# Optimization experiments

Measured on AMD Instinct MI355X. Metric: run time of the kernel, lower is better.

The kernel has to match this reference:

```python
import jax, jax.numpy as jnp
import numpy as np

N = 65536          # total nodes across batch
C = 256            # in channels
COUT = 256         # out channels
B = 8              # batch size (graphs)
EMB = 512          # emb channels
N_EDGE_TYPE = 7
N_NODE_TYPE = 7
AVG_DEGREE = 7
E = N * AVG_DEGREE
GROUP = 32         # min(32, channels)
EPS = 1e-5


def setup_inputs() -> dict:
    key = jax.random.key(0)
    ks = jax.random.split(key, 10)
    # GraphConv init: uniform xavier-like with fan scaled by avg_degree
    std = (2.0 / float(AVG_DEGREE * C + AVG_DEGREE * COUT)) ** 0.5
    a = (3.0 ** 0.5) * std
    return {
        "x": jax.random.normal(ks[0], (N, C), jnp.float32),
        "emb": jax.random.normal(ks[1], (B, EMB), jnp.float32),
        "batch_id": jnp.sort(jax.random.randint(ks[2], (N,), 0, B, jnp.int32)),
        "edge_index": jax.random.randint(ks[3], (2, E), 0, N, jnp.int32),
        "edge_type": jax.random.randint(ks[4], (E,), 0, N_EDGE_TYPE, jnp.int32),
        "node_type": jax.random.randint(ks[5], (N,), 0, N_NODE_TYPE, jnp.int32),
        "gn1_w": jnp.ones((1, C), jnp.float32),
        "gn1_b": jnp.zeros((1, C), jnp.float32),
        "conv1_w": jax.random.uniform(ks[6], (N_EDGE_TYPE * (C + N_NODE_TYPE), COUT), jnp.float32, -a, a),
        "emb_w": jax.random.normal(ks[7], (EMB, COUT), jnp.float32) * 0.02,
        "emb_b": jnp.zeros((COUT,), jnp.float32),
        "gn2_w": jnp.ones((1, COUT), jnp.float32),
        "gn2_b": jnp.zeros((1, COUT), jnp.float32),
        "conv2_w": jax.random.uniform(ks[8], (N_EDGE_TYPE * (COUT + N_NODE_TYPE), COUT), jnp.float32, -a, a),
    }


def _adjust_for_group(t, cpg):
    # sum stats within each group of cpg channels, broadcast back: [B, C]
    if cpg > 1:
        Bsz, Cn = t.shape
        g = Cn // cpg
        t = t.reshape(Bsz, g, cpg).sum(-1, keepdims=True)
        t = jnp.broadcast_to(t, (Bsz, g, cpg)).reshape(Bsz, Cn)
    return t


def dual_octree_group_norm(data, batch_id, w, b):
    # data: [N, C]; per-graph group norm via segment sums
    Cn = data.shape[1]
    cpg = Cn // GROUP
    ones = jnp.ones((data.shape[0], 1), data.dtype)
    count = jax.ops.segment_sum(ones, batch_id, num_segments=B) * cpg   # [B,1]
    inv_count = 1.0 / (count + EPS)
    mean = jax.ops.segment_sum(data, batch_id, num_segments=B) * inv_count
    mean = _adjust_for_group(mean, cpg)
    out = data - mean[batch_id]
    var = jax.ops.segment_sum(out * out, batch_id, num_segments=B) * inv_count
    var = _adjust_for_group(var, cpg)
    inv_std = 1.0 / jnp.sqrt(var + EPS)
    out = out * inv_std[batch_id]
    return out * w + b


def graph_conv(x, weights, edge_index, edge_type, node_type):
    # concat one-hot node type channels
    one_hot = jax.nn.one_hot(node_type, N_NODE_TYPE, dtype=x.dtype)
    xa = jnp.concatenate([x, one_hot], axis=1)          # [N, C+T]
    row, col = edge_index[0], edge_index[1]
    index = row * N_EDGE_TYPE + edge_type               # [E]
    col_data = jax.ops.segment_sum(xa[col], index, num_segments=xa.shape[0] * N_EDGE_TYPE)
    return col_data.reshape(xa.shape[0], -1) @ weights  # [N, COUT]


def reference(x, emb, batch_id, edge_index, edge_type, node_type,
              gn1_w, gn1_b, conv1_w, emb_w, emb_b, gn2_w, gn2_b, conv2_w):
    h = dual_octree_group_norm(x, batch_id, gn1_w, gn1_b)
    h = jax.nn.silu(h)
    h = graph_conv(h, conv1_w, edge_index, edge_type, node_type)
    emb_out = jax.nn.silu(emb) @ emb_w + emb_b          # [B, COUT]
    h = h + emb_out[batch_id]                           # per-batch add (loop in torch)
    h = dual_octree_group_norm(h, batch_id, gn2_w, gn2_b)
    h = jax.nn.silu(h)                                  # dropout p=0 -> identity
    h = graph_conv(h, conv2_w, edge_index, edge_type, node_type)
    return x + h                                        # skip is Identity (Cout==C)
```

## Files before the change

### kernel.cpp

```cpp
#include <hip/hip_runtime.h>
#include <math.h>

#define N_NODES 65536
#define B_GR    8
#define EMB_N   512
#define E_EDGES 458752
#define NSEG    458752
#define TSTRIDE 288
#define GK      2016
#define EPS     1e-5f

typedef unsigned short u16;
typedef unsigned int   u32;
typedef __bf16 bf16x8 __attribute__((ext_vector_type(8)));
typedef float  f32x4  __attribute__((ext_vector_type(4)));
typedef u16    u16x8  __attribute__((ext_vector_type(8)));

__device__ __forceinline__ float bf2f(u16 u) {
    u32 x = ((u32)u) << 16; float f; __builtin_memcpy(&f, &x, 4); return f;
}
__device__ __forceinline__ u16 f2bf(float f) {
    u32 x; __builtin_memcpy(&x, &f, 4);
    u32 r = x + 0x7fffu + ((x >> 16) & 1u);
    return (u16)(r >> 16);
}

__device__ __forceinline__ void stats_body(int nb, int tid, const float* __restrict__ xin,
                                           const int* __restrict__ batch_id,
                                           float* __restrict__ S, float* __restrict__ Q) {
    int c = tid;
    int n0 = nb * 64;
    float s = 0.f, q = 0.f;
    int bcur = batch_id[n0];
    for (int r = 0; r < 64; r++) {
        int n = n0 + r;
        int b = batch_id[n];
        if (b != bcur) {
            atomicAdd(&S[bcur * 256 + c], s);
            atomicAdd(&Q[bcur * 256 + c], q);
            s = 0.f; q = 0.f; bcur = b;
        }
        float v = xin[(size_t)n * 256 + c];
        s += v;
        q = fmaf(v, v, q);
    }
    atomicAdd(&S[bcur * 256 + c], s);
    atomicAdd(&Q[bcur * 256 + c], q);
}

__device__ __forceinline__ void norm_body(int nb, int tid, const float* __restrict__ xin,
                                          const int* __restrict__ batch_id,
                                          const float* __restrict__ S, const float* __restrict__ Q,
                                          const int* __restrict__ cnt,
                                          const float* __restrict__ w, const float* __restrict__ bias,
                                          u16* __restrict__ yout) {
    __shared__ float smean[256], sistd[256];
    {
        int b = tid >> 5, g = tid & 31;
        float Sg = 0.f, Qg = 0.f;
#pragma unroll
        for (int k = 0; k < 8; k++) {
            Sg += S[b * 256 + g * 8 + k];
            Qg += Q[b * 256 + g * 8 + k];
        }
        float cnt8 = (float)cnt[b] * 8.f;
        float D = cnt8 + EPS;
        float m = Sg / D;
        float var = (Qg - 2.f * m * Sg + cnt8 * m * m) / D;
        smean[tid] = m;
        sistd[tid] = rsqrtf(var + EPS);
    }
    __syncthreads();
    int n = nb * 8 + (tid >> 5);
    int g = tid & 31;
    int c0 = g * 8;
    int b = batch_id[n];
    float m = smean[b * 32 + g], is = sistd[b * 32 + g];
    u16x8 o;
#pragma unroll
    for (int k = 0; k < 8; k++) {
        float v = (xin[(size_t)n * 256 + c0 + k] - m) * is;
        v = v * w[c0 + k] + bias[c0 + k];
        v = v / (1.f + __expf(-v));
        o[k] = f2bf(v);
    }
    *(u16x8*)&yout[(size_t)n * 256 + c0] = o;
}

__global__ __launch_bounds__(256) void front_kernel(
    const int* __restrict__ batch_id, int* __restrict__ cnt,
    const float* __restrict__ w1, const float* __restrict__ w2,
    u16* __restrict__ Wt1, u16* __restrict__ Wt2,
    const float* __restrict__ emb, const float* __restrict__ embw,
    const float* __restrict__ embb, float* __restrict__ embout,
    const float* __restrict__ x, float* __restrict__ S, float* __restrict__ Q)
{
    int bid = blockIdx.x, tid = threadIdx.x;
    if (bid < 256) {
        int i = bid * 256 + tid;
        int b = batch_id[i];
#pragma unroll
        for (int bb = 0; bb < 8; bb++) {
            unsigned long long mm = __ballot(b == bb);
            if ((tid & 63) == 0 && mm) atomicAdd(&cnt[bb], (int)__popcll(mm));
        }
    } else if (bid < 1264) {
        int r = bid - 256;
        const float* Win = (r < 504) ? w1 : w2;
        u16* Wt = (r < 504) ? Wt1 : Wt2;
        r %= 504;
        int t  = r / 72;
        int r2 = r % 72;
        int cc0 = (r2 / 8) * 32;
        int n0  = (r2 % 8) * 32;
        __shared__ float tile[32][33];
        int cl = tid & 31, rh = tid >> 5;
#pragma unroll
        for (int rr = 0; rr < 4; rr++) {
            int c = cc0 + rh + rr * 8;
            float v = 0.f;
            if (c < 263) v = Win[(size_t)(t * 263 + c) * 256 + n0 + cl];
            tile[rh + rr * 8][cl] = v;
        }
        __syncthreads();
#pragma unroll
        for (int rr = 0; rr < 4; rr++) {
            int n = n0 + rh + rr * 8;
            Wt[(size_t)n * GK + t * TSTRIDE + cc0 + cl] = f2bf(tile[cl][rh + rr * 8]);
        }
    } else if (bid == 1264) {
        __shared__ float semb[B_GR * EMB_N];
        for (int i = tid; i < B_GR * EMB_N; i += 256) {
            float e = emb[i];
            semb[i] = e / (1.f + __expf(-e));
        }
        __syncthreads();
        float acc[8];
        float bb = embb[tid];
#pragma unroll
        for (int b = 0; b < 8; b++) acc[b] = bb;
        for (int k = 0; k < EMB_N; k++) {
            float wv = embw[k * 256 + tid];
#pragma unroll
            for (int b = 0; b < 8; b++) acc[b] += semb[b * EMB_N + k] * wv;
        }
#pragma unroll
        for (int b = 0; b < 8; b++) embout[b * 256 + tid] = acc[b];
    } else {
        stats_body(bid - 1265, tid, x, batch_id, S, Q);
    }
}

__global__ __launch_bounds__(256) void hist_norm_kernel(
    const int* __restrict__ ei, const int* __restrict__ et, int* __restrict__ hist,
    const float* __restrict__ xin, const int* __restrict__ batch_id,
    const float* __restrict__ S, const float* __restrict__ Q, const int* __restrict__ cnt,
    const float* __restrict__ w, const float* __restrict__ bias, u16* __restrict__ yout)
{
    int bid = blockIdx.x;
    if (bid < 1792) {
        int e = bid * 256 + threadIdx.x;
        int s = ei[e] * 7 + et[e];
        atomicAdd(&hist[s], 1);
    } else {
        norm_body(bid - 1792, threadIdx.x, xin, batch_id, S, Q, cnt, w, bias, yout);
    }
}

__global__ __launch_bounds__(256) void stats_kernel(const float* __restrict__ xin,
                                                    const int* __restrict__ batch_id,
                                                    float* __restrict__ S, float* __restrict__ Q) {
    stats_body(blockIdx.x, threadIdx.x, xin, batch_id, S, Q);
}
__global__ __launch_bounds__(256) void norm_kernel(const float* __restrict__ xin,
                                                   const int* __restrict__ batch_id,
                                                   const float* __restrict__ S, const float* __restrict__ Q,
                                                   const int* __restrict__ cnt,
                                                   const float* __restrict__ w, const float* __restrict__ bias,
                                                   u16* __restrict__ yout) {
    norm_body(blockIdx.x, threadIdx.x, xin, batch_id, S, Q, cnt, w, bias, yout);
}

__global__ __launch_bounds__(512) void scan1_kernel(const int* __restrict__ hist, int* __restrict__ partials) {
    __shared__ int sd[512];
    int i = blockIdx.x * 512 + threadIdx.x;
    sd[threadIdx.x] = hist[i];
    __syncthreads();
    for (int off = 256; off > 0; off >>= 1) {
        if (threadIdx.x < off) sd[threadIdx.x] += sd[threadIdx.x + off];
        __syncthreads();
    }
    if (threadIdx.x == 0) partials[blockIdx.x] = sd[0];
}

__global__ __launch_bounds__(1024) void scan2_kernel(int* __restrict__ partials) {
    __shared__ int sd[1024];
    int t = threadIdx.x;
    int v = (t < 896) ? partials[t] : 0;
    sd[t] = v;
    __syncthreads();
    for (int off = 1; off < 1024; off <<= 1) {
        int u = (t >= off) ? sd[t - off] : 0;
        __syncthreads();
        sd[t] += u;
        __syncthreads();
    }
    if (t < 896) partials[t] = sd[t] - v;
}

__global__ __launch_bounds__(512) void scan3_kernel(int* __restrict__ hist_offs, const int* __restrict__ partials,
                                                    int* __restrict__ cursor) {
    __shared__ int sd[512];
    int t = threadIdx.x;
    int i = blockIdx.x * 512 + t;
    int c = hist_offs[i];
    sd[t] = c;
    __syncthreads();
    for (int off = 1; off < 512; off <<= 1) {
        int u = (t >= off) ? sd[t - off] : 0;
        __syncthreads();
        sd[t] += u;
        __syncthreads();
    }
    int o = partials[blockIdx.x] + sd[t] - c;
    hist_offs[i] = o;
    cursor[i] = o;
}

__global__ __launch_bounds__(256) void fill_zero_kernel(const int* __restrict__ ei, const int* __restrict__ et,
                                                        int* __restrict__ cursor, int* __restrict__ elist,
                                                        float* __restrict__ S, float* __restrict__ Q) {
    int bid = blockIdx.x;
    if (bid < 1792) {
        int e = bid * 256 + threadIdx.x;
        int s = ei[e] * 7 + et[e];
        int p = atomicAdd(&cursor[s], 1);
        if (p >= 0 && p < E_EDGES) elist[p] = ei[E_EDGES + e];
    } else {
        int i = (bid - 1792) * 256 + threadIdx.x;
        S[i] = 0.f; Q[i] = 0.f;
    }
}

__global__ __launch_bounds__(512) void gemm_fused_kernel(
    const u16* __restrict__ y, const u16* __restrict__ Bt,
    const int* __restrict__ offs, const int* __restrict__ cursor,
    const int* __restrict__ elist, const int* __restrict__ node_type,
    const int* __restrict__ batch_id, const float* __restrict__ embout,
    const float* __restrict__ xres, float* __restrict__ out, int mode)
{
    __shared__ __align__(16) u16 As[2][64 * 64];
    int tid = threadIdx.x;
    int lane = tid & 63;
    int wn = tid >> 6;
    int lm = lane & 15, lq = lane >> 4;
    int m0 = blockIdx.x * 64;
    int ar = tid >> 3;
    int tq = tid & 7;

    f32x4 acc[4][2];
    f32x4 zz = {0.f, 0.f, 0.f, 0.f};
#pragma unroll
    for (int i = 0; i < 4; i++)
#pragma unroll
        for (int j = 0; j < 2; j++) acc[i][j] = zz;

    const u16* btp0 = Bt + (size_t)(wn * 32 + lm) * GK + lq * 8;
    const u16* btp1 = btp0 + (size_t)16 * GK;

    int sbase = (m0 + ar) * 7;

    int st = offs[sbase], en = cursor[sbase];
    int col[4];
#pragma unroll
    for (int u = 0; u < 4; u++) col[u] = (st + u < en) ? elist[st + u] : -1;
    u16x8 gv[4];
#pragma unroll
    for (int u = 0; u < 4; u++)
        if (col[u] >= 0) gv[u] = *(const u16x8*)&y[(size_t)col[u] * 256 + tq * 8];
    bf16x8 bcur[2][2];
#pragma unroll
    for (int k = 0; k < 2; k++) {
        bcur[k][0] = *(const bf16x8*)&btp0[k * 32];
        bcur[k][1] = *(const bf16x8*)&btp1[k * 32];
    }
    bf16x8 boh[2];
    int stn = 0, enn = 0;
    int coln[4] = {-1, -1, -1, -1};
    int nt4[4] = {-1, -1, -1, -1};
    int buf = 0;

    for (int t = 0; t < 7; t++) {
#pragma unroll
        for (int sc = 0; sc < 4; sc++) {
            float f[8];
#pragma unroll
            for (int j = 0; j < 8; j++) f[j] = 0.f;
#pragma unroll
            for (int u = 0; u < 4; u++)
                if (col[u] >= 0) {
#pragma unroll
                    for (int j = 0; j < 8; j++) f[j] += bf2f(gv[u][j]);
                }
            if (en - st > 4) {
                for (int e = st + 4; e < en; e++) {
                    u16x8 v = *(const u16x8*)&y[(size_t)elist[e] * 256 + sc * 64 + tq * 8];
#pragma unroll
                    for (int j = 0; j < 8; j++) f[j] += bf2f(v[j]);
                }
            }
            {
                u16x8 w8;
#pragma unroll
                for (int j = 0; j < 8; j++) w8[j] = f2bf(f[j]);
                *(u16x8*)&As[buf][ar * 64 + ((tq ^ (ar & 7)) * 8)] = w8;
            }
            __syncthreads();
            bf16x8 a[2][4];
#pragma unroll
            for (int k = 0; k < 2; k++)
#pragma unroll
                for (int i = 0; i < 4; i++) {
                    int row = i * 16 + lm;
                    a[k][i] = *(const bf16x8*)&As[buf][row * 64 + (((k * 4 + lq) ^ (row & 7)) * 8)];
                }
            bf16x8 bn00, bn01, bn10, bn11;
            if (sc < 3) {
                int cb = (sc + 1) * 64 + tq * 8;
#pragma unroll
                for (int u = 0; u < 4; u++)
                    if (col[u] >= 0) gv[u] = *(const u16x8*)&y[(size_t)col[u] * 256 + cb];
                int kb = t * TSTRIDE + (sc + 1) * 64;
                bn00 = *(const bf16x8*)&btp0[kb];
                bn01 = *(const bf16x8*)&btp1[kb];
                bn10 = *(const bf16x8*)&btp0[kb + 32];
                bn11 = *(const bf16x8*)&btp1[kb + 32];
                if (sc == 0 && t < 6) { stn = offs[sbase + t + 1]; enn = cursor[sbase + t + 1]; }
                if (sc == 1 && t < 6) {
#pragma unroll
                    for (int u = 0; u < 4; u++) coln[u] = (stn + u < enn) ? elist[stn + u] : -1;
                }
                if (sc == 2 && tq == 0) {
#pragma unroll
                    for (int u = 0; u < 4; u++) nt4[u] = (col[u] >= 0) ? node_type[col[u]] : -1;
                }
            } else {
                int kb = t * TSTRIDE + 256;
                boh[0] = *(const bf16x8*)&btp0[kb];
                boh[1] = *(const bf16x8*)&btp1[kb];
                if (t < 6) {
#pragma unroll
                    for (int u = 0; u < 4; u++)
                        if (coln[u] >= 0) gv[u] = *(const u16x8*)&y[(size_t)coln[u] * 256 + tq * 8];
                }
            }
            __builtin_amdgcn_s_setprio(1);
#pragma unroll
            for (int k = 0; k < 2; k++)
#pragma unroll
                for (int i = 0; i < 4; i++) {
                    acc[i][0] = __builtin_amdgcn_mfma_f32_16x16x32_bf16(a[k][i], bcur[k][0], acc[i][0], 0, 0, 0);
                    acc[i][1] = __builtin_amdgcn_mfma_f32_16x16x32_bf16(a[k][i], bcur[k][1], acc[i][1], 0, 0, 0);
                }
            __builtin_amdgcn_s_setprio(0);
            if (sc < 3) { bcur[0][0] = bn00; bcur[0][1] = bn01; bcur[1][0] = bn10; bcur[1][1] = bn11; }
            buf ^= 1;
        }
        {
            u16x8 w8;
#pragma unroll
            for (int j = 0; j < 8; j++) w8[j] = 0;
            if (tq == 0) {
                float oh[7];
#pragma unroll
                for (int j = 0; j < 7; j++)
                    oh[j] = (nt4[0] == j ? 1.f : 0.f) + (nt4[1] == j ? 1.f : 0.f)
                          + (nt4[2] == j ? 1.f : 0.f) + (nt4[3] == j ? 1.f : 0.f);
                if (en - st > 4) {
                    for (int e = st + 4; e < en; e++) {
                        int nt = node_type[elist[e]];
#pragma unroll
                        for (int j = 0; j < 7; j++) oh[j] += (nt == j) ? 1.f : 0.f;
                    }
                }
#pragma unroll
                for (int j = 0; j < 7; j++) w8[j] = f2bf(oh[j]);
            }
            *(u16x8*)&As[buf][ar * 64 + ((tq ^ (ar & 7)) * 8)] = w8;
            __syncthreads();
            bf16x8 a[4];
#pragma unroll
            for (int i = 0; i < 4; i++) {
                int row = i * 16 + lm;
                a[i] = *(const bf16x8*)&As[buf][row * 64 + ((lq ^ (row & 7)) * 8)];
            }
            if (t < 6) {
                int kb = (t + 1) * TSTRIDE;
                bcur[0][0] = *(const bf16x8*)&btp0[kb];
                bcur[0][1] = *(const bf16x8*)&btp1[kb];
                bcur[1][0] = *(const bf16x8*)&btp0[kb + 32];
                bcur[1][1] = *(const bf16x8*)&btp1[kb + 32];
            }
            __builtin_amdgcn_s_setprio(1);
#pragma unroll
            for (int i = 0; i < 4; i++) {
                acc[i][0] = __builtin_amdgcn_mfma_f32_16x16x32_bf16(a[i], boh[0], acc[i][0], 0, 0, 0);
                acc[i][1] = __builtin_amdgcn_mfma_f32_16x16x32_bf16(a[i], boh[1], acc[i][1], 0, 0, 0);
            }
            __builtin_amdgcn_s_setprio(0);
            st = stn; en = enn;
#pragma unroll
            for (int u = 0; u < 4; u++) col[u] = coln[u];
            buf ^= 1;
        }
    }

#pragma unroll
    for (int i = 0; i < 4; i++) {
#pragma unroll
        for (int r = 0; r < 4; r++) {
            size_t m = (size_t)m0 + i * 16 + lq * 4 + r;
            float addv[2];
            if (mode == 0) {
                int b = batch_id[m];
#pragma unroll
                for (int j = 0; j < 2; j++) addv[j] = embout[b * 256 + wn * 32 + j * 16 + lm];
            } else {
#pragma unroll
                for (int j = 0; j < 2; j++) addv[j] = xres[m * 256 + wn * 32 + j * 16 + lm];
            }
#pragma unroll
            for (int j = 0; j < 2; j++) {
                int n = wn * 32 + j * 16 + lm;
                out[m * 256 + n] = acc[i][j][r] + addv[j];
            }
        }
    }
}

extern "C" void kernel_launch(void* const* d_in, const int* in_sizes, int n_in,
                              void* d_out, int out_size, void* d_ws, size_t ws_size,
                              hipStream_t stream) {
    const float* x    = (const float*)d_in[0];
    const float* emb  = (const float*)d_in[1];
    const int* bid    = (const int*)d_in[2];
    const int* ei     = (const int*)d_in[3];
    const int* et     = (const int*)d_in[4];
    const int* ntp    = (const int*)d_in[5];
    const float* gn1w = (const float*)d_in[6];
    const float* gn1b = (const float*)d_in[7];
    const float* w1   = (const float*)d_in[8];
    const float* embw = (const float*)d_in[9];
    const float* embb = (const float*)d_in[10];
    const float* gn2w = (const float*)d_in[11];
    const float* gn2b = (const float*)d_in[12];
    const float* w2   = (const float*)d_in[13];
    float* out = (float*)d_out;

    char* p = (char*)d_ws;
    size_t off = 0;
    auto nxt = [&](size_t bytes) -> void* {
        void* r = p + off;
        off += (bytes + 255) & ~(size_t)255;
        return r;
    };
    u16*   y       = (u16*)nxt((size_t)N_NODES * 256 * 2);
    u16*   Wt1     = (u16*)nxt((size_t)256 * GK * 2);
    u16*   Wt2     = (u16*)nxt((size_t)256 * GK * 2);
    float* embout  = (float*)nxt(8 * 256 * 4);
    float* S       = (float*)nxt(2048 * 4);
    float* Q       = (float*)nxt(2048 * 4);
    int*   cnt     = (int*)nxt(8 * 4);
    int*   offs    = (int*)nxt((size_t)NSEG * 4);
    int*   cursor  = (int*)nxt((size_t)NSEG * 4);
    int*   parts   = (int*)nxt(1024 * 4);
    int*   elist   = (int*)nxt((size_t)E_EDGES * 4);
    float* h2      = out;
    (void)ws_size; (void)in_sizes; (void)n_in; (void)out_size;

    hipMemsetAsync(offs, 0, (size_t)NSEG * 4, stream);
    hipMemsetAsync(S, 0, 8192 + 8192 + 256, stream);
    front_kernel<<<2289, 256, 0, stream>>>(bid, cnt, w1, w2, Wt1, Wt2,
                                           emb, embw, embb, embout, x, S, Q);
    hist_norm_kernel<<<9984, 256, 0, stream>>>(ei, et, offs, x, bid, S, Q, cnt, gn1w, gn1b, y);
    scan1_kernel<<<896, 512, 0, stream>>>(offs, parts);
    scan2_kernel<<<1, 1024, 0, stream>>>(parts);
    scan3_kernel<<<896, 512, 0, stream>>>(offs, parts, cursor);
    fill_zero_kernel<<<1800, 256, 0, stream>>>(ei, et, cursor, elist, S, Q);
    gemm_fused_kernel<<<1024, 512, 0, stream>>>(y, Wt1, offs, cursor, elist, ntp, bid, embout, x, h2, 0);
    stats_kernel<<<1024, 256, 0, stream>>>(h2, bid, S, Q);
    norm_kernel<<<8192, 256, 0, stream>>>(h2, bid, S, Q, cnt, gn2w, gn2b, y);
    gemm_fused_kernel<<<1024, 512, 0, stream>>>(y, Wt2, offs, cursor, elist, ntp, bid, embout, x, out, 1);
}
```

Measured before the change: 749.6 us.

## Reorder graph conv as per-type GEMM followed by edge gather-sum

Instead of gathering neighbor features per (node, edge type) and then multiplying, first compute y times each edge-type weight block for all nodes into a large bf16 buffer, then gather-sum those projected rows per destination node. The one-hot node-type channels are written directly into a padded activation layout so the GEMM covers them. This targets the irregular gather inside the fused GEMM, trading it for a dense GEMM plus a large intermediate write and a random gather over it. The path is used only when the workspace is big enough, with the old fused kernel kept as a fallback.

```diff
diff --git a/kernel.cpp b/kernel.cpp
--- a/kernel.cpp
+++ b/kernel.cpp
@@ -8,6 +8,8 @@
 #define NSEG    458752
 #define TSTRIDE 288
 #define GK      2016
+#define YSTR    296
+#define ZN      1792
 #define EPS     1e-5f
 
 typedef unsigned short u16;
@@ -23,6 +25,10 @@
     u32 x; __builtin_memcpy(&x, &f, 4);
     u32 r = x + 0x7fffu + ((x >> 16) & 1u);
     return (u16)(r >> 16);
+}
+__device__ __forceinline__ void gload16(const u16* g, u16* l) {
+    __builtin_amdgcn_global_load_lds((const __attribute__((address_space(1))) void*)g,
+                                     (__attribute__((address_space(3))) void*)l, 16, 0, 0);
 }
 
 __device__ __forceinline__ void stats_body(int nb, int tid, const float* __restrict__ xin,
@@ -53,6 +59,7 @@
                                           const float* __restrict__ S, const float* __restrict__ Q,
                                           const int* __restrict__ cnt,
                                           const float* __restrict__ w, const float* __restrict__ bias,
+                                          const int* __restrict__ node_type,
                                           u16* __restrict__ yout) {
     __shared__ float smean[256], sistd[256];
     {
@@ -84,7 +91,18 @@
         v = v / (1.f + __expf(-v));
         o[k] = f2bf(v);
     }
-    *(u16x8*)&yout[(size_t)n * 256 + c0] = o;
+    *(u16x8*)&yout[(size_t)n * YSTR + c0] = o;
+    if (g < 4) {
+        u16x8 oh;
+#pragma unroll
+        for (int k = 0; k < 8; k++) oh[k] = 0;
+        if (g == 0) {
+            int nt = node_type[n];
+#pragma unroll
+            for (int k = 0; k < 7; k++) oh[k] = (nt == k) ? (u16)0x3F80 : (u16)0;
+        }
+        *(u16x8*)&yout[(size_t)n * YSTR + 256 + g * 8] = oh;
+    }
 }
 
 __global__ __launch_bounds__(256) void front_kernel(
@@ -93,7 +111,7 @@
     u16* __restrict__ Wt1, u16* __restrict__ Wt2,
     const float* __restrict__ emb, const float* __restrict__ embw,
     const float* __restrict__ embb, float* __restrict__ embout,
-    const float* __restrict__ x, float* __restrict__ S, float* __restrict__ Q)
+    const float* __restrict__ x, float* __restrict__ S, float* __restrict__ Q, int zmode)
 {
     int bid = blockIdx.x, tid = threadIdx.x;
     if (bid < 256) {
@@ -126,7 +144,11 @@
 #pragma unroll
         for (int rr = 0; rr < 4; rr++) {
             int n = n0 + rh + rr * 8;
-            Wt[(size_t)n * GK + t * TSTRIDE + cc0 + cl] = f2bf(tile[cl][rh + rr * 8]);
+            u16 v = f2bf(tile[cl][rh + rr * 8]);
+            if (zmode)
+                Wt[(size_t)(t * 256 + n) * 288 + cc0 + cl] = v;
+            else
+                Wt[(size_t)n * GK + t * TSTRIDE + cc0 + cl] = v;
         }
     } else if (bid == 1264) {
         __shared__ float semb[B_GR * EMB_N];
@@ -155,7 +177,8 @@
     const int* __restrict__ ei, const int* __restrict__ et, int* __restrict__ hist,
     const float* __restrict__ xin, const int* __restrict__ batch_id,
     const float* __restrict__ S, const float* __restrict__ Q, const int* __restrict__ cnt,
-    const float* __restrict__ w, const float* __restrict__ bias, u16* __restrict__ yout)
+    const float* __restrict__ w, const float* __restrict__ bias,
+    const int* __restrict__ node_type, u16* __restrict__ yout)
 {
     int bid = blockIdx.x;
     if (bid < 1792) {
@@ -163,7 +186,7 @@
         int s = ei[e] * 7 + et[e];
         atomicAdd(&hist[s], 1);
     } else {
-        norm_body(bid - 1792, threadIdx.x, xin, batch_id, S, Q, cnt, w, bias, yout);
+        norm_body(bid - 1792, threadIdx.x, xin, batch_id, S, Q, cnt, w, bias, node_type, yout);
     }
 }
 
@@ -177,8 +200,9 @@
                                                    const float* __restrict__ S, const float* __restrict__ Q,
                                                    const int* __restrict__ cnt,
                                                    const float* __restrict__ w, const float* __restrict__ bias,
+                                                   const int* __restrict__ node_type,
                                                    u16* __restrict__ yout) {
-    norm_body(blockIdx.x, threadIdx.x, xin, batch_id, S, Q, cnt, w, bias, yout);
+    norm_body(blockIdx.x, threadIdx.x, xin, batch_id, S, Q, cnt, w, bias, node_type, yout);
 }
 
 __global__ __launch_bounds__(512) void scan1_kernel(const int* __restrict__ hist, int* __restrict__ partials) {
@@ -229,17 +253,137 @@
 
 __global__ __launch_bounds__(256) void fill_zero_kernel(const int* __restrict__ ei, const int* __restrict__ et,
                                                         int* __restrict__ cursor, int* __restrict__ elist,
-                                                        float* __restrict__ S, float* __restrict__ Q) {
+                                                        float* __restrict__ S, float* __restrict__ Q, int pack) {
     int bid = blockIdx.x;
     if (bid < 1792) {
         int e = bid * 256 + threadIdx.x;
-        int s = ei[e] * 7 + et[e];
+        int t = et[e];
+        int s = ei[e] * 7 + t;
         int p = atomicAdd(&cursor[s], 1);
-        if (p >= 0 && p < E_EDGES) elist[p] = ei[E_EDGES + e];
+        int c = ei[E_EDGES + e];
+        if (p >= 0 && p < E_EDGES) elist[p] = pack ? (c * 7 + t) : c;
     } else {
         int i = (bid - 1792) * 256 + threadIdx.x;
         S[i] = 0.f; Q[i] = 0.f;
     }
+}
+
+__global__ __launch_bounds__(256) void zgemm_kernel(const u16* __restrict__ y,
+                                                    const u16* __restrict__ W,
+                                                    u16* __restrict__ z) {
+    __shared__ __align__(16) u16 As[64 * YSTR];
+    int tid = threadIdx.x;
+    int lane = tid & 63;
+    int wn = tid >> 6;
+    int lm = lane & 15, lq = lane >> 4;
+    int bid = blockIdx.x;
+    int wg = (bid & 7) * 896 + (bid >> 3);
+    int mblk = wg / 7, nblk = wg % 7;
+    int m0 = mblk * 64;
+
+    const u16* yg = y + (size_t)m0 * YSTR;
+#pragma unroll
+    for (int i = 0; i < 9; i++) {
+        int u = i * 256 + tid;
+        gload16(yg + (size_t)u * 8, &As[u * 8]);
+    }
+    if (tid < 64) {
+        int u = 2304 + tid;
+        gload16(yg + (size_t)u * 8, &As[u * 8]);
+    }
+
+    f32x4 acc[4][4];
+    f32x4 zz = {0.f, 0.f, 0.f, 0.f};
+#pragma unroll
+    for (int i = 0; i < 4; i++)
+#pragma unroll
+        for (int j = 0; j < 4; j++) acc[i][j] = zz;
+    const u16* bp = W + (size_t)(nblk * 256 + wn * 64 + lm) * 288 + lq * 8;
+
+    __syncthreads();
+
+    bf16x8 bc[4], bn[4];
+#pragma unroll
+    for (int j = 0; j < 4; j++) bc[j] = *(const bf16x8*)&bp[j * 4608];
+
+#pragma unroll
+    for (int ph = 0; ph < 9; ph++) {
+        bf16x8 a[4];
+#pragma unroll
+        for (int i = 0; i < 4; i++)
+            a[i] = *(const bf16x8*)&As[(i * 16 + lm) * YSTR + ph * 32 + lq * 8];
+        if (ph < 8) {
+#pragma unroll
+            for (int j = 0; j < 4; j++) bn[j] = *(const bf16x8*)&bp[j * 4608 + (ph + 1) * 32];
+        }
+        __builtin_amdgcn_s_setprio(1);
+#pragma unroll
+        for (int i = 0; i < 4; i++)
+#pragma unroll
+            for (int j = 0; j < 4; j++)
+                acc[i][j] = __builtin_amdgcn_mfma_f32_16x16x32_bf16(a[i], bc[j], acc[i][j], 0, 0, 0);
+        __builtin_amdgcn_s_setprio(0);
+        if (ph < 8) {
+#pragma unroll
+            for (int j = 0; j < 4; j++) bc[j] = bn[j];
+        }
+    }
+
+    __syncthreads();
+#pragma unroll
+    for (int i = 0; i < 4; i++)
+#pragma unroll
+        for (int r = 0; r < 4; r++) {
+            int row = i * 16 + lq * 4 + r;
+#pragma unroll
+            for (int j = 0; j < 4; j++)
+                As[row * 256 + wn * 64 + j * 16 + lm] = f2bf(acc[i][j][r]);
+        }
+    __syncthreads();
+#pragma unroll
+    for (int k = 0; k < 8; k++) {
+        int u = k * 256 + tid;
+        int ru = u >> 5, cu = u & 31;
+        *(u16x8*)&z[((size_t)m0 + ru) * ZN + nblk * 256 + cu * 8] =
+            *(const u16x8*)&As[ru * 256 + cu * 8];
+    }
+}
+
+__global__ __launch_bounds__(256) void scatter_kernel(const u16* __restrict__ z,
+        const int* __restrict__ offs, const int* __restrict__ cursor,
+        const int* __restrict__ elist, const int* __restrict__ batch_id,
+        const float* __restrict__ embout, const float* __restrict__ xres,
+        float* __restrict__ out, int mode) {
+    int tid = threadIdx.x;
+    int r = blockIdx.x * 8 + (tid >> 5);
+    int oct = tid & 31;
+    int st = offs[r * 7];
+    int en = cursor[r * 7 + 6];
+    float a0[8], a1[8];
+#pragma unroll
+    for (int j = 0; j < 8; j++) { a0[j] = 0.f; a1[j] = 0.f; }
+    int e = st;
+    for (; e + 2 <= en; e += 2) {
+        int i0 = elist[e], i1 = elist[e + 1];
+        u16x8 v0 = *(const u16x8*)&z[(size_t)i0 * 256 + oct * 8];
+        u16x8 v1 = *(const u16x8*)&z[(size_t)i1 * 256 + oct * 8];
+#pragma unroll
+        for (int j = 0; j < 8; j++) { a0[j] += bf2f(v0[j]); a1[j] += bf2f(v1[j]); }
+    }
+    if (e < en) {
+        u16x8 v0 = *(const u16x8*)&z[(size_t)elist[e] * 256 + oct * 8];
+#pragma unroll
+        for (int j = 0; j < 8; j++) a0[j] += bf2f(v0[j]);
+    }
+    const float* ap = (mode == 0) ? &embout[batch_id[r] * 256 + oct * 8]
+                                  : &xres[(size_t)r * 256 + oct * 8];
+    f32x4 o0, o1;
+#pragma unroll
+    for (int j = 0; j < 4; j++) o0[j] = a0[j] + a1[j] + ap[j];
+#pragma unroll
+    for (int j = 0; j < 4; j++) o1[j] = a0[4 + j] + a1[4 + j] + ap[4 + j];
+    *(f32x4*)&out[(size_t)r * 256 + oct * 8] = o0;
+    *(f32x4*)&out[(size_t)r * 256 + oct * 8 + 4] = o1;
 }
 
 __global__ __launch_bounds__(512) void gemm_fused_kernel(
@@ -269,7 +413,6 @@
     const u16* btp1 = btp0 + (size_t)16 * GK;
 
     int sbase = (m0 + ar) * 7;
-
     int st = offs[sbase], en = cursor[sbase];
     int col[4];
 #pragma unroll
@@ -277,7 +420,7 @@
     u16x8 gv[4];
 #pragma unroll
     for (int u = 0; u < 4; u++)
-        if (col[u] >= 0) gv[u] = *(const u16x8*)&y[(size_t)col[u] * 256 + tq * 8];
+        if (col[u] >= 0) gv[u] = *(const u16x8*)&y[(size_t)col[u] * YSTR + tq * 8];
     bf16x8 bcur[2][2];
 #pragma unroll
     for (int k = 0; k < 2; k++) {
@@ -304,7 +447,7 @@
                 }
             if (en - st > 4) {
                 for (int e = st + 4; e < en; e++) {
-                    u16x8 v = *(const u16x8*)&y[(size_t)elist[e] * 256 + sc * 64 + tq * 8];
+                    u16x8 v = *(const u16x8*)&y[(size_t)elist[e] * YSTR + sc * 64 + tq * 8];
 #pragma unroll
                     for (int j = 0; j < 8; j++) f[j] += bf2f(v[j]);
                 }
@@ -329,7 +472,7 @@
                 int cb = (sc + 1) * 64 + tq * 8;
 #pragma unroll
                 for (int u = 0; u < 4; u++)
-                    if (col[u] >= 0) gv[u] = *(const u16x8*)&y[(size_t)col[u] * 256 + cb];
+                    if (col[u] >= 0) gv[u] = *(const u16x8*)&y[(size_t)col[u] * YSTR + cb];
                 int kb = t * TSTRIDE + (sc + 1) * 64;
                 bn00 = *(const bf16x8*)&btp0[kb];
                 bn01 = *(const bf16x8*)&btp1[kb];
@@ -351,7 +494,7 @@
                 if (t < 6) {
 #pragma unroll
                     for (int u = 0; u < 4; u++)
-                        if (coln[u] >= 0) gv[u] = *(const u16x8*)&y[(size_t)coln[u] * 256 + tq * 8];
+                        if (coln[u] >= 0) gv[u] = *(const u16x8*)&y[(size_t)coln[u] * YSTR + tq * 8];
                 }
             }
             __builtin_amdgcn_s_setprio(1);
@@ -464,9 +607,9 @@
         off += (bytes + 255) & ~(size_t)255;
         return r;
     };
-    u16*   y       = (u16*)nxt((size_t)N_NODES * 256 * 2);
-    u16*   Wt1     = (u16*)nxt((size_t)256 * GK * 2);
-    u16*   Wt2     = (u16*)nxt((size_t)256 * GK * 2);
+    u16*   y       = (u16*)nxt((size_t)N_NODES * YSTR * 2);
+    u16*   Wt1     = (u16*)nxt((size_t)ZN * 288 * 2);
+    u16*   Wt2     = (u16*)nxt((size_t)ZN * 288 * 2);
     float* embout  = (float*)nxt(8 * 256 * 4);
     float* S       = (float*)nxt(2048 * 4);
     float* Q       = (float*)nxt(2048 * 4);
@@ -475,20 +618,32 @@
     int*   cursor  = (int*)nxt((size_t)NSEG * 4);
     int*   parts   = (int*)nxt(1024 * 4);
     int*   elist   = (int*)nxt((size_t)E_EDGES * 4);
+    u16*   z       = (u16*)nxt((size_t)N_NODES * ZN * 2);
     float* h2      = out;
-    (void)ws_size; (void)in_sizes; (void)n_in; (void)out_size;
+    int split = (off <= ws_size) ? 1 : 0;
+    (void)in_sizes; (void)n_in; (void)out_size;
 
     hipMemsetAsync(offs, 0, (size_t)NSEG * 4, stream);
-    hipMemsetAsync(S, 0, 8192 + 8192 + 256, stream);
+    hipMemsetAsync(S, 0, 16416, stream);
     front_kernel<<<2289, 256, 0, stream>>>(bid, cnt, w1, w2, Wt1, Wt2,
-                                           emb, embw, embb, embout, x, S, Q);
-    hist_norm_kernel<<<9984, 256, 0, stream>>>(ei, et, offs, x, bid, S, Q, cnt, gn1w, gn1b, y);
+                                           emb, embw, embb, embout, x, S, Q, split);
+    hist_norm_kernel<<<9984, 256, 0, stream>>>(ei, et, offs, x, bid, S, Q, cnt, gn1w, gn1b, ntp, y);
     scan1_kernel<<<896, 512, 0, stream>>>(offs, parts);
     scan2_kernel<<<1, 1024, 0, stream>>>(parts);
     scan3_kernel<<<896, 512, 0, stream>>>(offs, parts, cursor);
-    fill_zero_kernel<<<1800, 256, 0, stream>>>(ei, et, cursor, elist, S, Q);
-    gemm_fused_kernel<<<1024, 512, 0, stream>>>(y, Wt1, offs, cursor, elist, ntp, bid, embout, x, h2, 0);
-    stats_kernel<<<1024, 256, 0, stream>>>(h2, bid, S, Q);
-    norm_kernel<<<8192, 256, 0, stream>>>(h2, bid, S, Q, cnt, gn2w, gn2b, y);
-    gemm_fused_kernel<<<1024, 512, 0, stream>>>(y, Wt2, offs, cursor, elist, ntp, bid, embout, x, out, 1);
-}
+    fill_zero_kernel<<<1800, 256, 0, stream>>>(ei, et, cursor, elist, S, Q, split);
+
+    if (split) {
+        zgemm_kernel<<<7168, 256, 0, stream>>>(y, Wt1, z);
+        scatter_kernel<<<8192, 256, 0, stream>>>(z, offs, cursor, elist, bid, embout, x, h2, 0);
+        stats_kernel<<<1024, 256, 0, stream>>>(h2, bid, S, Q);
+        norm_kernel<<<8192, 256, 0, stream>>>(h2, bid, S, Q, cnt, gn2w, gn2b, ntp, y);
+        zgemm_kernel<<<7168, 256, 0, stream>>>(y, Wt2, z);
+        scatter_kernel<<<8192, 256, 0, stream>>>(z, offs, cursor, elist, bid, embout, x, out, 1);
+    } else {
+        gemm_fused_kernel<<<1024, 512, 0, stream>>>(y, Wt1, offs, cursor, elist, ntp, bid, embout, x, h2, 0);
+        stats_kernel<<<1024, 256, 0, stream>>>(h2, bid, S, Q);
+        norm_kernel<<<8192, 256, 0, stream>>>(h2, bid, S, Q, cnt, gn2w, gn2b, ntp, y);
+        gemm_fused_kernel<<<1024, 512, 0, stream>>>(y, Wt2, offs, cursor, elist, ntp, bid, embout, x, out, 1);
+    }
+}
```

Measured after the change: 755.0 us. About the same (+0.7%).

## Store one-hot node types in padded activation rows and gather them with features

Applied to the files above, without the earlier changes.

The normalization kernels now write bf16 activations with a padded row stride of 296. The one-hot node-type channels go in the extra columns, so the fused gather-GEMM reads them as a fifth K slice. This replaces the separate node_type lookups and per-edge one-hot counting inside the GEMM. The pipeline is also restructured to prefetch neighbor feature chunks two stages ahead with a gvA/gvB double buffer, and to spread B-tile loads across five substeps. The cost is extra bytes per node row (padding plus the zero one-hot tail written by four threads) and a fifth sync per edge type.

```diff
diff --git a/kernel.cpp b/kernel.cpp
--- a/kernel.cpp
+++ b/kernel.cpp
@@ -8,6 +8,7 @@
 #define NSEG    458752
 #define TSTRIDE 288
 #define GK      2016
+#define YSTR    296
 #define EPS     1e-5f
 
 typedef unsigned short u16;
@@ -53,6 +54,7 @@
                                           const float* __restrict__ S, const float* __restrict__ Q,
                                           const int* __restrict__ cnt,
                                           const float* __restrict__ w, const float* __restrict__ bias,
+                                          const int* __restrict__ node_type,
                                           u16* __restrict__ yout) {
     __shared__ float smean[256], sistd[256];
     {
@@ -84,7 +86,18 @@
         v = v / (1.f + __expf(-v));
         o[k] = f2bf(v);
     }
-    *(u16x8*)&yout[(size_t)n * 256 + c0] = o;
+    *(u16x8*)&yout[(size_t)n * YSTR + c0] = o;
+    if (g < 4) {
+        u16x8 oh;
+#pragma unroll
+        for (int k = 0; k < 8; k++) oh[k] = 0;
+        if (g == 0) {
+            int nt = node_type[n];
+#pragma unroll
+            for (int k = 0; k < 7; k++) oh[k] = (nt == k) ? (u16)0x3F80 : (u16)0;
+        }
+        *(u16x8*)&yout[(size_t)n * YSTR + 256 + g * 8] = oh;
+    }
 }
 
 __global__ __launch_bounds__(256) void front_kernel(
@@ -155,7 +168,8 @@
     const int* __restrict__ ei, const int* __restrict__ et, int* __restrict__ hist,
     const float* __restrict__ xin, const int* __restrict__ batch_id,
     const float* __restrict__ S, const float* __restrict__ Q, const int* __restrict__ cnt,
-    const float* __restrict__ w, const float* __restrict__ bias, u16* __restrict__ yout)
+    const float* __restrict__ w, const float* __restrict__ bias,
+    const int* __restrict__ node_type, u16* __restrict__ yout)
 {
     int bid = blockIdx.x;
     if (bid < 1792) {
@@ -163,7 +177,7 @@
         int s = ei[e] * 7 + et[e];
         atomicAdd(&hist[s], 1);
     } else {
-        norm_body(bid - 1792, threadIdx.x, xin, batch_id, S, Q, cnt, w, bias, yout);
+        norm_body(bid - 1792, threadIdx.x, xin, batch_id, S, Q, cnt, w, bias, node_type, yout);
     }
 }
 
@@ -177,8 +191,9 @@
                                                    const float* __restrict__ S, const float* __restrict__ Q,
                                                    const int* __restrict__ cnt,
                                                    const float* __restrict__ w, const float* __restrict__ bias,
+                                                   const int* __restrict__ node_type,
                                                    u16* __restrict__ yout) {
-    norm_body(blockIdx.x, threadIdx.x, xin, batch_id, S, Q, cnt, w, bias, yout);
+    norm_body(blockIdx.x, threadIdx.x, xin, batch_id, S, Q, cnt, w, bias, node_type, yout);
 }
 
 __global__ __launch_bounds__(512) void scan1_kernel(const int* __restrict__ hist, int* __restrict__ partials) {
@@ -245,7 +260,7 @@
 __global__ __launch_bounds__(512) void gemm_fused_kernel(
     const u16* __restrict__ y, const u16* __restrict__ Bt,
     const int* __restrict__ offs, const int* __restrict__ cursor,
-    const int* __restrict__ elist, const int* __restrict__ node_type,
+    const int* __restrict__ elist,
     const int* __restrict__ batch_id, const float* __restrict__ embout,
     const float* __restrict__ xres, float* __restrict__ out, int mode)
 {
@@ -257,6 +272,7 @@
     int m0 = blockIdx.x * 64;
     int ar = tid >> 3;
     int tq = tid & 7;
+    int oq = tq & 3;
 
     f32x4 acc[4][2];
     f32x4 zz = {0.f, 0.f, 0.f, 0.f};
@@ -274,25 +290,26 @@
     int col[4];
 #pragma unroll
     for (int u = 0; u < 4; u++) col[u] = (st + u < en) ? elist[st + u] : -1;
-    u16x8 gv[4];
+    u16x8 gvA[4], gvB[4];
 #pragma unroll
     for (int u = 0; u < 4; u++)
-        if (col[u] >= 0) gv[u] = *(const u16x8*)&y[(size_t)col[u] * 256 + tq * 8];
+        if (col[u] >= 0) gvA[u] = *(const u16x8*)&y[(size_t)col[u] * YSTR + tq * 8];
+#pragma unroll
+    for (int u = 0; u < 4; u++)
+        if (col[u] >= 0) gvB[u] = *(const u16x8*)&y[(size_t)col[u] * YSTR + 64 + tq * 8];
+
     bf16x8 bcur[2][2];
-#pragma unroll
-    for (int k = 0; k < 2; k++) {
-        bcur[k][0] = *(const bf16x8*)&btp0[k * 32];
-        bcur[k][1] = *(const bf16x8*)&btp1[k * 32];
-    }
-    bf16x8 boh[2];
-    int stn = 0, enn = 0;
-    int coln[4] = {-1, -1, -1, -1};
-    int nt4[4] = {-1, -1, -1, -1};
+    bcur[0][0] = *(const bf16x8*)&btp0[0];
+    bcur[0][1] = *(const bf16x8*)&btp1[0];
+    bcur[1][0] = *(const bf16x8*)&btp0[32];
+    bcur[1][1] = *(const bf16x8*)&btp1[32];
+
+    int nst = 0, nen = 0, ncol[4] = {-1, -1, -1, -1};
     int buf = 0;
 
     for (int t = 0; t < 7; t++) {
 #pragma unroll
-        for (int sc = 0; sc < 4; sc++) {
+        for (int sc = 0; sc < 5; sc++) {
             float f[8];
 #pragma unroll
             for (int j = 0; j < 8; j++) f[j] = 0.f;
@@ -300,11 +317,12 @@
             for (int u = 0; u < 4; u++)
                 if (col[u] >= 0) {
 #pragma unroll
-                    for (int j = 0; j < 8; j++) f[j] += bf2f(gv[u][j]);
+                    for (int j = 0; j < 8; j++) f[j] += bf2f(gvA[u][j]);
                 }
             if (en - st > 4) {
+                int cb = (sc == 4) ? (256 + oq * 8) : (sc * 64 + tq * 8);
                 for (int e = st + 4; e < en; e++) {
-                    u16x8 v = *(const u16x8*)&y[(size_t)elist[e] * 256 + sc * 64 + tq * 8];
+                    u16x8 v = *(const u16x8*)&y[(size_t)elist[e] * YSTR + cb];
 #pragma unroll
                     for (int j = 0; j < 8; j++) f[j] += bf2f(v[j]);
                 }
@@ -313,104 +331,96 @@
                 u16x8 w8;
 #pragma unroll
                 for (int j = 0; j < 8; j++) w8[j] = f2bf(f[j]);
-                *(u16x8*)&As[buf][ar * 64 + ((tq ^ (ar & 7)) * 8)] = w8;
+                int slot = (sc == 4) ? (oq ^ (ar & 7)) : (tq ^ (ar & 7));
+                *(u16x8*)&As[buf][ar * 64 + slot * 8] = w8;
             }
             __syncthreads();
-            bf16x8 a[2][4];
-#pragma unroll
-            for (int k = 0; k < 2; k++)
-#pragma unroll
-                for (int i = 0; i < 4; i++) {
-                    int row = i * 16 + lm;
-                    a[k][i] = *(const bf16x8*)&As[buf][row * 64 + (((k * 4 + lq) ^ (row & 7)) * 8)];
-                }
-            bf16x8 bn00, bn01, bn10, bn11;
-            if (sc < 3) {
-                int cb = (sc + 1) * 64 + tq * 8;
-#pragma unroll
-                for (int u = 0; u < 4; u++)
-                    if (col[u] >= 0) gv[u] = *(const u16x8*)&y[(size_t)col[u] * 256 + cb];
-                int kb = t * TSTRIDE + (sc + 1) * 64;
-                bn00 = *(const bf16x8*)&btp0[kb];
-                bn01 = *(const bf16x8*)&btp1[kb];
-                bn10 = *(const bf16x8*)&btp0[kb + 32];
-                bn11 = *(const bf16x8*)&btp1[kb + 32];
-                if (sc == 0 && t < 6) { stn = offs[sbase + t + 1]; enn = cursor[sbase + t + 1]; }
-                if (sc == 1 && t < 6) {
-#pragma unroll
-                    for (int u = 0; u < 4; u++) coln[u] = (stn + u < enn) ? elist[stn + u] : -1;
-                }
-                if (sc == 2 && tq == 0) {
-#pragma unroll
-                    for (int u = 0; u < 4; u++) nt4[u] = (col[u] >= 0) ? node_type[col[u]] : -1;
-                }
-            } else {
-                int kb = t * TSTRIDE + 256;
-                boh[0] = *(const bf16x8*)&btp0[kb];
-                boh[1] = *(const bf16x8*)&btp1[kb];
-                if (t < 6) {
-#pragma unroll
-                    for (int u = 0; u < 4; u++)
-                        if (coln[u] >= 0) gv[u] = *(const u16x8*)&y[(size_t)coln[u] * 256 + tq * 8];
-                }
-            }
-            __builtin_amdgcn_s_setprio(1);
-#pragma unroll
-            for (int k = 0; k < 2; k++)
-#pragma unroll
-                for (int i = 0; i < 4; i++) {
-                    acc[i][0] = __builtin_amdgcn_mfma_f32_16x16x32_bf16(a[k][i], bcur[k][0], acc[i][0], 0, 0, 0);
-                    acc[i][1] = __builtin_amdgcn_mfma_f32_16x16x32_bf16(a[k][i], bcur[k][1], acc[i][1], 0, 0, 0);
-                }
-            __builtin_amdgcn_s_setprio(0);
-            if (sc < 3) { bcur[0][0] = bn00; bcur[0][1] = bn01; bcur[1][0] = bn10; bcur[1][1] = bn11; }
-            buf ^= 1;
-        }
-        {
-            u16x8 w8;
-#pragma unroll
-            for (int j = 0; j < 8; j++) w8[j] = 0;
-            if (tq == 0) {
-                float oh[7];
-#pragma unroll
-                for (int j = 0; j < 7; j++)
-                    oh[j] = (nt4[0] == j ? 1.f : 0.f) + (nt4[1] == j ? 1.f : 0.f)
-                          + (nt4[2] == j ? 1.f : 0.f) + (nt4[3] == j ? 1.f : 0.f);
-                if (en - st > 4) {
-                    for (int e = st + 4; e < en; e++) {
-                        int nt = node_type[elist[e]];
-#pragma unroll
-                        for (int j = 0; j < 7; j++) oh[j] += (nt == j) ? 1.f : 0.f;
-                    }
-                }
-#pragma unroll
-                for (int j = 0; j < 7; j++) w8[j] = f2bf(oh[j]);
-            }
-            *(u16x8*)&As[buf][ar * 64 + ((tq ^ (ar & 7)) * 8)] = w8;
-            __syncthreads();
-            bf16x8 a[4];
+            bf16x8 a0[4], a1[4];
 #pragma unroll
             for (int i = 0; i < 4; i++) {
                 int row = i * 16 + lm;
-                a[i] = *(const bf16x8*)&As[buf][row * 64 + ((lq ^ (row & 7)) * 8)];
-            }
-            if (t < 6) {
-                int kb = (t + 1) * TSTRIDE;
-                bcur[0][0] = *(const bf16x8*)&btp0[kb];
-                bcur[0][1] = *(const bf16x8*)&btp1[kb];
-                bcur[1][0] = *(const bf16x8*)&btp0[kb + 32];
-                bcur[1][1] = *(const bf16x8*)&btp1[kb + 32];
+                a0[i] = *(const bf16x8*)&As[buf][row * 64 + ((lq ^ (row & 7)) * 8)];
+                if (sc < 4)
+                    a1[i] = *(const bf16x8*)&As[buf][row * 64 + (((4 + lq) ^ (row & 7)) * 8)];
+            }
+            bf16x8 bn00, bn01, bn10, bn11;
+            if (sc == 0) {
+                int cb = 128 + tq * 8;
+#pragma unroll
+                for (int u = 0; u < 4; u++)
+                    if (col[u] >= 0) gvA[u] = *(const u16x8*)&y[(size_t)col[u] * YSTR + cb];
+                if (t < 6) { nst = offs[sbase + t + 1]; nen = cursor[sbase + t + 1]; }
+                int kb = t * TSTRIDE + 64;
+                bn00 = *(const bf16x8*)&btp0[kb];      bn01 = *(const bf16x8*)&btp1[kb];
+                bn10 = *(const bf16x8*)&btp0[kb + 32]; bn11 = *(const bf16x8*)&btp1[kb + 32];
+            } else if (sc == 1) {
+                int cb = 192 + tq * 8;
+#pragma unroll
+                for (int u = 0; u < 4; u++)
+                    if (col[u] >= 0) gvA[u] = *(const u16x8*)&y[(size_t)col[u] * YSTR + cb];
+                if (t < 6) {
+#pragma unroll
+                    for (int u = 0; u < 4; u++) ncol[u] = (nst + u < nen) ? elist[nst + u] : -1;
+                }
+                int kb = t * TSTRIDE + 128;
+                bn00 = *(const bf16x8*)&btp0[kb];      bn01 = *(const bf16x8*)&btp1[kb];
+                bn10 = *(const bf16x8*)&btp0[kb + 32]; bn11 = *(const bf16x8*)&btp1[kb + 32];
+            } else if (sc == 2) {
+                int cb = 256 + oq * 8;
+#pragma unroll
+                for (int u = 0; u < 4; u++)
+                    if (col[u] >= 0) gvA[u] = *(const u16x8*)&y[(size_t)col[u] * YSTR + cb];
+                int kb = t * TSTRIDE + 192;
+                bn00 = *(const bf16x8*)&btp0[kb];      bn01 = *(const bf16x8*)&btp1[kb];
+                bn10 = *(const bf16x8*)&btp0[kb + 32]; bn11 = *(const bf16x8*)&btp1[kb + 32];
+            } else if (sc == 3) {
+                if (t < 6) {
+                    int cb = tq * 8;
+#pragma unroll
+                    for (int u = 0; u < 4; u++)
+                        if (ncol[u] >= 0) gvA[u] = *(const u16x8*)&y[(size_t)ncol[u] * YSTR + cb];
+                }
+                int kb = t * TSTRIDE + 256;
+                bn00 = *(const bf16x8*)&btp0[kb];      bn01 = *(const bf16x8*)&btp1[kb];
+            } else {
+                if (t < 6) {
+                    int cb = 64 + tq * 8;
+#pragma unroll
+                    for (int u = 0; u < 4; u++)
+                        if (ncol[u] >= 0) gvA[u] = *(const u16x8*)&y[(size_t)ncol[u] * YSTR + cb];
+                    int kb = (t + 1) * TSTRIDE;
+                    bn00 = *(const bf16x8*)&btp0[kb];      bn01 = *(const bf16x8*)&btp1[kb];
+                    bn10 = *(const bf16x8*)&btp0[kb + 32]; bn11 = *(const bf16x8*)&btp1[kb + 32];
+                }
             }
             __builtin_amdgcn_s_setprio(1);
 #pragma unroll
             for (int i = 0; i < 4; i++) {
-                acc[i][0] = __builtin_amdgcn_mfma_f32_16x16x32_bf16(a[i], boh[0], acc[i][0], 0, 0, 0);
-                acc[i][1] = __builtin_amdgcn_mfma_f32_16x16x32_bf16(a[i], boh[1], acc[i][1], 0, 0, 0);
+                acc[i][0] = __builtin_amdgcn_mfma_f32_16x16x32_bf16(a0[i], bcur[0][0], acc[i][0], 0, 0, 0);
+                acc[i][1] = __builtin_amdgcn_mfma_f32_16x16x32_bf16(a0[i], bcur[0][1], acc[i][1], 0, 0, 0);
+            }
+            if (sc < 4) {
+#pragma unroll
+                for (int i = 0; i < 4; i++) {
+                    acc[i][0] = __builtin_amdgcn_mfma_f32_16x16x32_bf16(a1[i], bcur[1][0], acc[i][0], 0, 0, 0);
+                    acc[i][1] = __builtin_amdgcn_mfma_f32_16x16x32_bf16(a1[i], bcur[1][1], acc[i][1], 0, 0, 0);
+                }
             }
             __builtin_amdgcn_s_setprio(0);
-            st = stn; en = enn;
-#pragma unroll
-            for (int u = 0; u < 4; u++) col[u] = coln[u];
+            if (sc == 3) {
+                bcur[0][0] = bn00; bcur[0][1] = bn01;
+            } else if (sc == 4) {
+                if (t < 6) { bcur[0][0] = bn00; bcur[0][1] = bn01; bcur[1][0] = bn10; bcur[1][1] = bn11; }
+            } else {
+                bcur[0][0] = bn00; bcur[0][1] = bn01; bcur[1][0] = bn10; bcur[1][1] = bn11;
+            }
+#pragma unroll
+            for (int u = 0; u < 4; u++) { u16x8 tmp = gvA[u]; gvA[u] = gvB[u]; gvB[u] = tmp; }
+            if (sc == 4) {
+                st = nst; en = nen;
+#pragma unroll
+                for (int u = 0; u < 4; u++) col[u] = ncol[u];
+            }
             buf ^= 1;
         }
     }
@@ -464,7 +474,7 @@
         off += (bytes + 255) & ~(size_t)255;
         return r;
     };
-    u16*   y       = (u16*)nxt((size_t)N_NODES * 256 * 2);
+    u16*   y       = (u16*)nxt((size_t)N_NODES * YSTR * 2);
     u16*   Wt1     = (u16*)nxt((size_t)256 * GK * 2);
     u16*   Wt2     = (u16*)nxt((size_t)256 * GK * 2);
     float* embout  = (float*)nxt(8 * 256 * 4);
@@ -479,16 +489,16 @@
     (void)ws_size; (void)in_sizes; (void)n_in; (void)out_size;
 
     hipMemsetAsync(offs, 0, (size_t)NSEG * 4, stream);
-    hipMemsetAsync(S, 0, 8192 + 8192 + 256, stream);
+    hipMemsetAsync(S, 0, 16416, stream);
     front_kernel<<<2289, 256, 0, stream>>>(bid, cnt, w1, w2, Wt1, Wt2,
                                            emb, embw, embb, embout, x, S, Q);
-    hist_norm_kernel<<<9984, 256, 0, stream>>>(ei, et, offs, x, bid, S, Q, cnt, gn1w, gn1b, y);
+    hist_norm_kernel<<<9984, 256, 0, stream>>>(ei, et, offs, x, bid, S, Q, cnt, gn1w, gn1b, ntp, y);
     scan1_kernel<<<896, 512, 0, stream>>>(offs, parts);
     scan2_kernel<<<1, 1024, 0, stream>>>(parts);
     scan3_kernel<<<896, 512, 0, stream>>>(offs, parts, cursor);
     fill_zero_kernel<<<1800, 256, 0, stream>>>(ei, et, cursor, elist, S, Q);
-    gemm_fused_kernel<<<1024, 512, 0, stream>>>(y, Wt1, offs, cursor, elist, ntp, bid, embout, x, h2, 0);
+    gemm_fused_kernel<<<1024, 512, 0, stream>>>(y, Wt1, offs, cursor, elist, bid, embout, x, h2, 0);
     stats_kernel<<<1024, 256, 0, stream>>>(h2, bid, S, Q);
-    norm_kernel<<<8192, 256, 0, stream>>>(h2, bid, S, Q, cnt, gn2w, gn2b, y);
-    gemm_fused_kernel<<<1024, 512, 0, stream>>>(y, Wt2, offs, cursor, elist, ntp, bid, embout, x, out, 1);
-}
+    norm_kernel<<<8192, 256, 0, stream>>>(h2, bid, S, Q, cnt, gn2w, gn2b, ntp, y);
+    gemm_fused_kernel<<<1024, 512, 0, stream>>>(y, Wt2, offs, cursor, elist, bid, embout, x, out, 1);
+}
```

After: 736.2 us. Within noise of the previous version (-1.8%).
